# Kernel optimization log

Measured on AMD Instinct MI355X. Metric: run time of the kernel, lower is better.

## Reference

```python
import jax, jax.numpy as jnp
import numpy as np

M, K, N = 8192, 4096, 4096

def setup_inputs() -> dict:
    key = jax.random.key(0)
    k1, k2, k3, k4, k5 = jax.random.split(key, 5)
    # int8-range quantized tensors stored as int32 (int8 values in [-128, 127])
    inp = jax.random.randint(k1, (M, K), -128, 128, dtype=jnp.int32)
    weight = jax.random.randint(k2, (N, K), -128, 128, dtype=jnp.int32)
    bias = jax.random.normal(k3, (N,), dtype=jnp.float32)
    inp_scales = jax.random.uniform(k4, (1,), jnp.float32, 0.01, 0.05)        # per-tensor
    inp_zero_points = jnp.zeros((1,), jnp.int32)                               # symmetric
    weight_scales = jax.random.uniform(k5, (N,), jnp.float32, 0.005, 0.02)     # per-channel
    weight_zero_points = jnp.zeros((N,), jnp.int32)
    return {
        "inp": inp, "weight": weight, "bias": bias,
        "inp_scales": inp_scales, "inp_zero_points": inp_zero_points,
        "weight_scales": weight_scales, "weight_zero_points": weight_zero_points,
    }

def reference(inp, weight, bias, inp_scales, inp_zero_points, weight_scales, weight_zero_points):
    # qdq_linear fallback path: dequantize activation (per-tensor) and weight
    # (per-output-channel), fp32 matmul, add bias. output_dtype=float32,
    # output_scales/zero_points=None => no output requantization.
    x = (inp.astype(jnp.float32) - inp_zero_points.astype(jnp.float32)) * inp_scales  # [M,K]
    w = (weight.astype(jnp.float32) - weight_zero_points[:, None].astype(jnp.float32)) \
        * weight_scales[:, None]                                                      # [N,K]
    return jnp.einsum('mk,nk->mn', x, w) + bias                                       # [M,N]
```

## Files before the change

### kernel.cpp

```cpp
#include <hip/hip_runtime.h>

#define MM 8192
#define NN 4096
#define KK 4096

#define BM 256
#define BN 256
#define BK 64
#define NT (KK / BK)
#define SLOT_BYTES 32768
#define B_OFF 16384

typedef int int32x4  __attribute__((ext_vector_type(4)));
typedef int int32x16 __attribute__((ext_vector_type(16)));

__device__ __forceinline__ void async_load16(const void* g, void* l) {
  __builtin_amdgcn_global_load_lds(
      (__attribute__((address_space(1))) void*)(void*)g,
      (__attribute__((address_space(3))) void*)l,
      16, 0, 0);
}

__global__ __launch_bounds__(256) void pack_kernel(
    const int* __restrict__ a, const int* __restrict__ w,
    char* __restrict__ a8, char* __restrict__ w8,
    const int* __restrict__ izp, const int* __restrict__ wzp) {
  const long tid = (long)blockIdx.x * 256 + threadIdx.x;
  const long A_T = (long)MM * KK / 16;

  const int4* src;
  int4* dst;
  int z;
  if (tid < A_T) {
    src = (const int4*)a + tid * 4;
    dst = (int4*)a8 + tid;
    z = izp[0];
  } else {
    const long t = tid - A_T;
    src = (const int4*)w + t * 4;
    dst = (int4*)w8 + t;
    z = wzp[t >> 8];
  }

  int4 v0 = src[0], v1 = src[1], v2 = src[2], v3 = src[3];
  union { char c[16]; int4 q; } u;
  u.c[0]  = (char)(v0.x - z); u.c[1]  = (char)(v0.y - z);
  u.c[2]  = (char)(v0.z - z); u.c[3]  = (char)(v0.w - z);
  u.c[4]  = (char)(v1.x - z); u.c[5]  = (char)(v1.y - z);
  u.c[6]  = (char)(v1.z - z); u.c[7]  = (char)(v1.w - z);
  u.c[8]  = (char)(v2.x - z); u.c[9]  = (char)(v2.y - z);
  u.c[10] = (char)(v2.z - z); u.c[11] = (char)(v2.w - z);
  u.c[12] = (char)(v3.x - z); u.c[13] = (char)(v3.y - z);
  u.c[14] = (char)(v3.z - z); u.c[15] = (char)(v3.w - z);
  *dst = u.q;
}

__global__ __launch_bounds__(512, 2) void qgemm_kernel(
    const char* __restrict__ A8, const char* __restrict__ W8,
    float* __restrict__ out,
    const float* __restrict__ bias,
    const float* __restrict__ is_ptr,
    const float* __restrict__ wscale) {
  __shared__ __attribute__((aligned(16))) char lds[4 * SLOT_BYTES];

  int pid = blockIdx.x;
  pid = (pid & 7) * 64 + (pid >> 3);
  const int bm = pid >> 4;
  const int bn = pid & 15;

  const int tid  = threadIdx.x;
  const int wid  = tid >> 6;
  const int lane = tid & 63;
  const int wm = (wid >> 2) * 128;
  const int wn = (wid & 3) * 64;

  const int srow = lane >> 2;
  const int ssub = (lane & 3) ^ ((lane >> 3) & 3);
  const char* a_src[2];
  const char* b_src[2];
  int c_off[2];
#pragma unroll
  for (int i = 0; i < 2; ++i) {
    const int c = wid + i * 8;
    a_src[i] = A8 + (long)(bm * BM + c * 16 + srow) * KK + ssub * 16;
    b_src[i] = W8 + (long)(bn * BN + c * 16 + srow) * KK + ssub * 16;
    c_off[i] = c * 1024;
  }

#define STAGE_A(I, T) \
  async_load16(a_src[I] + (T) * BK, lds + ((T) & 3) * SLOT_BYTES + c_off[I])
#define STAGE_B(I, T) \
  async_load16(b_src[I] + (T) * BK, lds + ((T) & 3) * SLOT_BYTES + B_OFF + c_off[I])

  const int r31 = lane & 31;
  const int hi  = lane >> 5;
  const int rx  = (r31 >> 1) & 3;
  const int ps0 = ((0 + hi) ^ rx) * 16;
  const int ps1 = ((2 + hi) ^ rx) * 16;
  const int a_row = (wm + r31) * BK;
  const int b_row = (wn + r31) * BK;

  int32x16 acc[4][2];
#pragma unroll
  for (int mi = 0; mi < 4; ++mi)
#pragma unroll
    for (int ni = 0; ni < 2; ++ni) acc[mi][ni] = (int32x16)0;

#pragma unroll
  for (int t0 = 0; t0 < 3; ++t0) {
    STAGE_A(0, t0); STAGE_A(1, t0);
    STAGE_B(0, t0); STAGE_B(1, t0);
  }

#define PHASE(PS, SB, STAGE_STMT)                                            \
  {                                                                          \
    const char* ar_ = lds + (SB) + a_row;                                    \
    const char* br_ = lds + (SB) + B_OFF + b_row;                            \
    int32x4 af0 = *(const int32x4*)(ar_ + 0 * 32 * BK + (PS));               \
    int32x4 af1 = *(const int32x4*)(ar_ + 1 * 32 * BK + (PS));               \
    int32x4 af2 = *(const int32x4*)(ar_ + 2 * 32 * BK + (PS));               \
    int32x4 af3 = *(const int32x4*)(ar_ + 3 * 32 * BK + (PS));               \
    int32x4 bf0 = *(const int32x4*)(br_ + 0 * 32 * BK + (PS));               \
    int32x4 bf1 = *(const int32x4*)(br_ + 1 * 32 * BK + (PS));               \
    STAGE_STMT;                                                              \
    __builtin_amdgcn_s_setprio(1);                                           \
    acc[0][0] = __builtin_amdgcn_mfma_i32_32x32x32_i8(af0, bf0, acc[0][0], 0, 0, 0); \
    acc[0][1] = __builtin_amdgcn_mfma_i32_32x32x32_i8(af0, bf1, acc[0][1], 0, 0, 0); \
    acc[1][0] = __builtin_amdgcn_mfma_i32_32x32x32_i8(af1, bf0, acc[1][0], 0, 0, 0); \
    acc[1][1] = __builtin_amdgcn_mfma_i32_32x32x32_i8(af1, bf1, acc[1][1], 0, 0, 0); \
    acc[2][0] = __builtin_amdgcn_mfma_i32_32x32x32_i8(af2, bf0, acc[2][0], 0, 0, 0); \
    acc[2][1] = __builtin_amdgcn_mfma_i32_32x32x32_i8(af2, bf1, acc[2][1], 0, 0, 0); \
    acc[3][0] = __builtin_amdgcn_mfma_i32_32x32x32_i8(af3, bf0, acc[3][0], 0, 0, 0); \
    acc[3][1] = __builtin_amdgcn_mfma_i32_32x32x32_i8(af3, bf1, acc[3][1], 0, 0, 0); \
    __builtin_amdgcn_s_setprio(0);                                           \
  }

#pragma unroll 4
  for (int t = 0; t < NT; ++t) {
    const int sb = (t & 3) * SLOT_BYTES;
    asm volatile("s_waitcnt vmcnt(8)" ::: "memory");
    __builtin_amdgcn_s_barrier();
    PHASE(ps0, sb, if (t < NT - 3) { STAGE_A(0, t + 3); STAGE_A(1, t + 3); })
    PHASE(ps1, sb, if (t < NT - 3) { STAGE_B(0, t + 3); STAGE_B(1, t + 3); })
  }

  const float is0 = is_ptr[0];
  const int row_base = bm * BM + wm + 4 * hi;
  const int col_base = bn * BN + wn + r31;
#pragma unroll
  for (int ni = 0; ni < 2; ++ni) {
    const int col = col_base + ni * 32;
    const float s = is0 * wscale[col];
    const float b = bias[col];
#pragma unroll
    for (int mi = 0; mi < 4; ++mi) {
      const long rb = (long)(row_base + mi * 32) * NN + col;
#pragma unroll
      for (int r = 0; r < 16; ++r) {
        const int roff = (r & 3) + 8 * (r >> 2);
        out[rb + (long)roff * NN] = (float)acc[mi][ni][r] * s + b;
      }
    }
  }
#undef PHASE
#undef STAGE_A
#undef STAGE_B
}

extern "C" void kernel_launch(void* const* d_in, const int* in_sizes, int n_in,
                              void* d_out, int out_size, void* d_ws, size_t ws_size,
                              hipStream_t stream) {
  const int*   inp    = (const int*)d_in[0];
  const int*   weight = (const int*)d_in[1];
  const float* bias   = (const float*)d_in[2];
  const float* iscale = (const float*)d_in[3];
  const int*   izp    = (const int*)d_in[4];
  const float* wscale = (const float*)d_in[5];
  const int*   wzp    = (const int*)d_in[6];
  float* out = (float*)d_out;

  char* a8 = (char*)d_ws;
  char* w8 = a8 + (size_t)MM * KK;

  pack_kernel<<<12288, 256, 0, stream>>>(inp, weight, a8, w8, izp, wzp);

  qgemm_kernel<<<512, 512, 0, stream>>>(a8, w8, out, bias, iscale, wscale);
}
```

Baseline: 404.3 us.

## Use 4-wave 128x128 warp tiles with register double-buffered fragments

The GEMM goes from 8 waves with 128x64 warp tiles to 4 waves with 128x128 warp tiles (16 MFMAs per fragment set). LDS fragment reads are double-buffered in registers so reads for the next half-step overlap MFMAs, and sched_barriers pin the order. The K loop is peeled into a steady state plus an explicit tail. The pack kernel now has each thread handle 4 ints instead of 16. The larger accumulator footprint (256 VGPRs of accumulators) may cause spills or leave too little latency hiding with only 4 waves per block.

Result: no change. 402.3 us (-0.5%).

```diff
diff --git a/kernel.cpp b/kernel.cpp
--- a/kernel.cpp
+++ b/kernel.cpp
@@ -8,8 +8,8 @@
 #define BN 256
 #define BK 64
 #define NT (KK / BK)
-#define SLOT_BYTES 32768
-#define B_OFF 16384
+#define A_BYTES (BM * BK)
+#define SLOT 32768
 
 typedef int int32x4  __attribute__((ext_vector_type(4)));
 typedef int int32x16 __attribute__((ext_vector_type(16)));
@@ -26,42 +26,38 @@
     char* __restrict__ a8, char* __restrict__ w8,
     const int* __restrict__ izp, const int* __restrict__ wzp) {
   const long tid = (long)blockIdx.x * 256 + threadIdx.x;
-  const long A_T = (long)MM * KK / 16;
+  const long A_T = (long)MM * KK / 4;
 
   const int4* src;
-  int4* dst;
+  int* dst;
   int z;
   if (tid < A_T) {
-    src = (const int4*)a + tid * 4;
-    dst = (int4*)a8 + tid;
+    src = (const int4*)a + tid;
+    dst = (int*)a8 + tid;
     z = izp[0];
   } else {
-    const long t = tid - A_T;
-    src = (const int4*)w + t * 4;
-    dst = (int4*)w8 + t;
-    z = wzp[t >> 8];
-  }
-
-  int4 v0 = src[0], v1 = src[1], v2 = src[2], v3 = src[3];
-  union { char c[16]; int4 q; } u;
-  u.c[0]  = (char)(v0.x - z); u.c[1]  = (char)(v0.y - z);
-  u.c[2]  = (char)(v0.z - z); u.c[3]  = (char)(v0.w - z);
-  u.c[4]  = (char)(v1.x - z); u.c[5]  = (char)(v1.y - z);
-  u.c[6]  = (char)(v1.z - z); u.c[7]  = (char)(v1.w - z);
-  u.c[8]  = (char)(v2.x - z); u.c[9]  = (char)(v2.y - z);
-  u.c[10] = (char)(v2.z - z); u.c[11] = (char)(v2.w - z);
-  u.c[12] = (char)(v3.x - z); u.c[13] = (char)(v3.y - z);
-  u.c[14] = (char)(v3.z - z); u.c[15] = (char)(v3.w - z);
+    long t = tid - A_T;
+    src = (const int4*)w + t;
+    dst = (int*)w8 + t;
+    z = wzp[t >> 10];
+  }
+
+  int4 v = *src;
+  union { char c[4]; int q; } u;
+  u.c[0] = (char)(v.x - z);
+  u.c[1] = (char)(v.y - z);
+  u.c[2] = (char)(v.z - z);
+  u.c[3] = (char)(v.w - z);
   *dst = u.q;
 }
 
-__global__ __launch_bounds__(512, 2) void qgemm_kernel(
+__global__ __launch_bounds__(256, 1) void qgemm_kernel(
     const char* __restrict__ A8, const char* __restrict__ W8,
     float* __restrict__ out,
     const float* __restrict__ bias,
     const float* __restrict__ is_ptr,
     const float* __restrict__ wscale) {
-  __shared__ __attribute__((aligned(16))) char lds[4 * SLOT_BYTES];
+  __shared__ __attribute__((aligned(16))) char lds[4 * SLOT];
 
   int pid = blockIdx.x;
   pid = (pid & 7) * 64 + (pid >> 3);
@@ -71,26 +67,34 @@
   const int tid  = threadIdx.x;
   const int wid  = tid >> 6;
   const int lane = tid & 63;
-  const int wm = (wid >> 2) * 128;
-  const int wn = (wid & 3) * 64;
+  const int wm = (wid & 1) * 128;
+  const int wn = (wid >> 1) * 128;
 
   const int srow = lane >> 2;
   const int ssub = (lane & 3) ^ ((lane >> 3) & 3);
-  const char* a_src[2];
-  const char* b_src[2];
-  int c_off[2];
-#pragma unroll
-  for (int i = 0; i < 2; ++i) {
-    const int c = wid + i * 8;
+  const char* a_src[4];
+  const char* b_src[4];
+  int c_off[4];
+#pragma unroll
+  for (int i = 0; i < 4; ++i) {
+    const int c = wid + i * 4;
     a_src[i] = A8 + (long)(bm * BM + c * 16 + srow) * KK + ssub * 16;
     b_src[i] = W8 + (long)(bn * BN + c * 16 + srow) * KK + ssub * 16;
     c_off[i] = c * 1024;
   }
 
-#define STAGE_A(I, T) \
-  async_load16(a_src[I] + (T) * BK, lds + ((T) & 3) * SLOT_BYTES + c_off[I])
-#define STAGE_B(I, T) \
-  async_load16(b_src[I] + (T) * BK, lds + ((T) & 3) * SLOT_BYTES + B_OFF + c_off[I])
+#define STAGE8(T)                                                            \
+  {                                                                          \
+    char* sl_ = lds + ((T) & 3) * SLOT;                                      \
+    async_load16(a_src[0] + (T) * BK, sl_ + c_off[0]);                       \
+    async_load16(a_src[1] + (T) * BK, sl_ + c_off[1]);                       \
+    async_load16(a_src[2] + (T) * BK, sl_ + c_off[2]);                       \
+    async_load16(a_src[3] + (T) * BK, sl_ + c_off[3]);                       \
+    async_load16(b_src[0] + (T) * BK, sl_ + A_BYTES + c_off[0]);             \
+    async_load16(b_src[1] + (T) * BK, sl_ + A_BYTES + c_off[1]);             \
+    async_load16(b_src[2] + (T) * BK, sl_ + A_BYTES + c_off[2]);             \
+    async_load16(b_src[3] + (T) * BK, sl_ + A_BYTES + c_off[3]);             \
+  }
 
   const int r31 = lane & 31;
   const int hi  = lane >> 5;
@@ -100,55 +104,98 @@
   const int a_row = (wm + r31) * BK;
   const int b_row = (wn + r31) * BK;
 
-  int32x16 acc[4][2];
+#define READ8(AF, BF, T, PS)                                                 \
+  {                                                                          \
+    const char* ar_ = lds + ((T) & 3) * SLOT + a_row;                        \
+    const char* br_ = lds + ((T) & 3) * SLOT + A_BYTES + b_row;              \
+    AF[0] = *(const int32x4*)(ar_ + 0 * 2048 + (PS));                        \
+    AF[1] = *(const int32x4*)(ar_ + 1 * 2048 + (PS));                        \
+    AF[2] = *(const int32x4*)(ar_ + 2 * 2048 + (PS));                        \
+    AF[3] = *(const int32x4*)(ar_ + 3 * 2048 + (PS));                        \
+    BF[0] = *(const int32x4*)(br_ + 0 * 2048 + (PS));                        \
+    BF[1] = *(const int32x4*)(br_ + 1 * 2048 + (PS));                        \
+    BF[2] = *(const int32x4*)(br_ + 2 * 2048 + (PS));                        \
+    BF[3] = *(const int32x4*)(br_ + 3 * 2048 + (PS));                        \
+  }
+
+  int32x16 acc[4][4];
 #pragma unroll
   for (int mi = 0; mi < 4; ++mi)
 #pragma unroll
-    for (int ni = 0; ni < 2; ++ni) acc[mi][ni] = (int32x16)0;
-
-#pragma unroll
-  for (int t0 = 0; t0 < 3; ++t0) {
-    STAGE_A(0, t0); STAGE_A(1, t0);
-    STAGE_B(0, t0); STAGE_B(1, t0);
-  }
-
-#define PHASE(PS, SB, STAGE_STMT)                                            \
-  {                                                                          \
-    const char* ar_ = lds + (SB) + a_row;                                    \
-    const char* br_ = lds + (SB) + B_OFF + b_row;                            \
-    int32x4 af0 = *(const int32x4*)(ar_ + 0 * 32 * BK + (PS));               \
-    int32x4 af1 = *(const int32x4*)(ar_ + 1 * 32 * BK + (PS));               \
-    int32x4 af2 = *(const int32x4*)(ar_ + 2 * 32 * BK + (PS));               \
-    int32x4 af3 = *(const int32x4*)(ar_ + 3 * 32 * BK + (PS));               \
-    int32x4 bf0 = *(const int32x4*)(br_ + 0 * 32 * BK + (PS));               \
-    int32x4 bf1 = *(const int32x4*)(br_ + 1 * 32 * BK + (PS));               \
-    STAGE_STMT;                                                              \
-    __builtin_amdgcn_s_setprio(1);                                           \
-    acc[0][0] = __builtin_amdgcn_mfma_i32_32x32x32_i8(af0, bf0, acc[0][0], 0, 0, 0); \
-    acc[0][1] = __builtin_amdgcn_mfma_i32_32x32x32_i8(af0, bf1, acc[0][1], 0, 0, 0); \
-    acc[1][0] = __builtin_amdgcn_mfma_i32_32x32x32_i8(af1, bf0, acc[1][0], 0, 0, 0); \
-    acc[1][1] = __builtin_amdgcn_mfma_i32_32x32x32_i8(af1, bf1, acc[1][1], 0, 0, 0); \
-    acc[2][0] = __builtin_amdgcn_mfma_i32_32x32x32_i8(af2, bf0, acc[2][0], 0, 0, 0); \
-    acc[2][1] = __builtin_amdgcn_mfma_i32_32x32x32_i8(af2, bf1, acc[2][1], 0, 0, 0); \
-    acc[3][0] = __builtin_amdgcn_mfma_i32_32x32x32_i8(af3, bf0, acc[3][0], 0, 0, 0); \
-    acc[3][1] = __builtin_amdgcn_mfma_i32_32x32x32_i8(af3, bf1, acc[3][1], 0, 0, 0); \
-    __builtin_amdgcn_s_setprio(0);                                           \
-  }
+    for (int ni = 0; ni < 4; ++ni) acc[mi][ni] = (int32x16)0;
+
+  int32x4 aC[4], bC[4];
+  int32x4 aN[4], bN[4];
+
+#define MFMA16(AF, BF)                                                       \
+  {                                                                          \
+    _Pragma("unroll")                                                        \
+    for (int mi = 0; mi < 4; ++mi)                                           \
+      _Pragma("unroll")                                                      \
+      for (int ni = 0; ni < 4; ++ni)                                         \
+        acc[mi][ni] = __builtin_amdgcn_mfma_i32_32x32x32_i8(                 \
+            AF[mi], BF[ni], acc[mi][ni], 0, 0, 0);                           \
+  }
+
+#define SBAR() __builtin_amdgcn_sched_barrier(0)
+
+#define FULL_BODY(T)                                                         \
+  {                                                                          \
+    STAGE8((T) + 3);                                                         \
+    READ8(aN, bN, (T), ps1);                                                 \
+    SBAR();                                                                  \
+    MFMA16(aC, bC);                                              \
+    SBAR();                                                                  \
+    READ8(aC, bC, (T) + 1, ps0);                                             \
+    SBAR();                                                                  \
+    MFMA16(aN, bN);                                              \
+    SBAR();                                                                  \
+    asm volatile("s_waitcnt vmcnt(8)" ::: "memory");                         \
+    __builtin_amdgcn_s_barrier();                                            \
+  }
+
+  STAGE8(0);
+  STAGE8(1);
+  STAGE8(2);
+  asm volatile("s_waitcnt vmcnt(8)" ::: "memory");
+  __builtin_amdgcn_s_barrier();
+  READ8(aC, bC, 0, ps0);
 
 #pragma unroll 4
-  for (int t = 0; t < NT; ++t) {
-    const int sb = (t & 3) * SLOT_BYTES;
-    asm volatile("s_waitcnt vmcnt(8)" ::: "memory");
-    __builtin_amdgcn_s_barrier();
-    PHASE(ps0, sb, if (t < NT - 3) { STAGE_A(0, t + 3); STAGE_A(1, t + 3); })
-    PHASE(ps1, sb, if (t < NT - 3) { STAGE_B(0, t + 3); STAGE_B(1, t + 3); })
-  }
+  for (int t = 0; t < 60; ++t) {
+    FULL_BODY(t);
+  }
+  FULL_BODY(60);
+  asm volatile("s_waitcnt vmcnt(0)" ::: "memory");
+  __builtin_amdgcn_s_barrier();
+
+  READ8(aN, bN, 61, ps1);
+  SBAR();
+  MFMA16(aC, bC);
+  SBAR();
+  READ8(aC, bC, 62, ps0);
+  SBAR();
+  MFMA16(aN, bN);
+  SBAR();
+  READ8(aN, bN, 62, ps1);
+  SBAR();
+  MFMA16(aC, bC);
+  SBAR();
+  READ8(aC, bC, 63, ps0);
+  SBAR();
+  MFMA16(aN, bN);
+  SBAR();
+  READ8(aN, bN, 63, ps1);
+  SBAR();
+  MFMA16(aC, bC);
+  SBAR();
+  MFMA16(aN, bN);
 
   const float is0 = is_ptr[0];
   const int row_base = bm * BM + wm + 4 * hi;
   const int col_base = bn * BN + wn + r31;
 #pragma unroll
-  for (int ni = 0; ni < 2; ++ni) {
+  for (int ni = 0; ni < 4; ++ni) {
     const int col = col_base + ni * 32;
     const float s = is0 * wscale[col];
     const float b = bias[col];
@@ -162,9 +209,11 @@
       }
     }
   }
-#undef PHASE
-#undef STAGE_A
-#undef STAGE_B
+#undef FULL_BODY
+#undef SBAR
+#undef MFMA16
+#undef READ8
+#undef STAGE8
 }
 
 extern "C" void kernel_launch(void* const* d_in, const int* in_sizes, int n_in,
@@ -182,7 +231,7 @@
   char* a8 = (char*)d_ws;
   char* w8 = a8 + (size_t)MM * KK;
 
-  pack_kernel<<<12288, 256, 0, stream>>>(inp, weight, a8, w8, izp, wzp);
-
-  qgemm_kernel<<<512, 512, 0, stream>>>(a8, w8, out, bias, iscale, wscale);
-}
+  pack_kernel<<<49152, 256, 0, stream>>>(inp, weight, a8, w8, izp, wzp);
+
+  qgemm_kernel<<<512, 256, 0, stream>>>(a8, w8, out, bias, iscale, wscale);
+}
```
